# Optimization experiments

Hardware: AMD Instinct MI355X
Metric: run time of the kernel (lower is better)

Reference implementation:

```python
import jax, jax.numpy as jnp
import numpy as np

N_QUESTION = 10000
B, S = 256, 500
Q_DIM = 128
QA_DIM = 128
M = 64            # memory_size
KEY_DIM = 128
VAL_DIM = 256


def setup_inputs() -> dict:
    key = jax.random.key(0)
    ks = jax.random.split(key, 10)
    q_data = jax.random.randint(ks[0], (B, S), 0, N_QUESTION + 1)
    qa_data = jax.random.randint(ks[1], (B, S), 0, 2 * N_QUESTION + 1)
    # embedding tables with padding_idx=0 zeroed
    q_embed_w = jax.random.normal(ks[2], (N_QUESTION + 1, Q_DIM), jnp.float32) * 0.05
    q_embed_w = q_embed_w.at[0].set(0.0)
    qa_embed_w = jax.random.normal(ks[3], (2 * N_QUESTION + 1, QA_DIM), jnp.float32) * 0.05
    qa_embed_w = qa_embed_w.at[0].set(0.0)
    key_mem = jax.random.normal(ks[4], (M, KEY_DIM), jnp.float32) * (2.0 / KEY_DIM) ** 0.5
    init_value_mem = jax.random.normal(ks[5], (M, VAL_DIM), jnp.float32) * (2.0 / VAL_DIM) ** 0.5
    erase_W = jax.random.normal(ks[6], (QA_DIM, VAL_DIM), jnp.float32) * (2.0 / QA_DIM) ** 0.5
    erase_b = jnp.zeros((VAL_DIM,), jnp.float32)
    add_W = jax.random.normal(ks[7], (QA_DIM, VAL_DIM), jnp.float32) * (2.0 / QA_DIM) ** 0.5
    add_b = jnp.zeros((VAL_DIM,), jnp.float32)
    return {
        "q_data": q_data, "qa_data": qa_data,
        "q_embed_w": q_embed_w, "qa_embed_w": qa_embed_w,
        "key_mem": key_mem, "init_value_mem": init_value_mem,
        "erase_W": erase_W, "erase_b": erase_b,
        "add_W": add_W, "add_b": add_b,
    }


def reference(q_data, qa_data, q_embed_w, qa_embed_w, key_mem, init_value_mem,
              erase_W, erase_b, add_W, add_b):
    q_emb = q_embed_w[q_data]     # [B,S,Qd]
    qa_emb = qa_embed_w[qa_data]  # [B,S,QAd]
    write_mask = (q_data >= 1).astype(jnp.float32)  # [B,S]

    Mv0 = jnp.broadcast_to(init_value_mem[None], (q_data.shape[0], M, VAL_DIM))

    def step(Mv, xs):
        q_t, qa_t, m_t = xs  # [B,Qd], [B,QAd], [B]
        # attention over memory slots
        w = jax.nn.softmax(q_t @ key_mem.T, axis=-1)           # [B,M]
        read = jnp.einsum('bm,bmd->bd', w, Mv)                 # [B,D]
        erase = jax.nn.sigmoid(qa_t @ erase_W + erase_b)       # [B,D]
        add = jnp.tanh(qa_t @ add_W + add_b)                   # [B,D]
        new_Mv = Mv * (1.0 - w[:, :, None] * erase[:, None, :]) \
                 + w[:, :, None] * add[:, None, :]
        Mv = jnp.where(m_t[:, None, None] > 0, new_Mv, Mv)
        return Mv, read

    xs = (jnp.swapaxes(q_emb, 0, 1), jnp.swapaxes(qa_emb, 0, 1),
          jnp.swapaxes(write_mask, 0, 1))
    _, reads = jax.lax.scan(step, Mv0, xs)        # reads: [S,B,D]
    reads = jnp.swapaxes(reads, 0, 1)             # [B,S,D]
    # shift right by one timestep, zero-pad first step
    out = jnp.concatenate([jnp.zeros_like(reads[:, :1]), reads[:, :-1]], axis=1)
    return out
```

## Files before the change

kernel.cpp:

```cpp
#include <hip/hip_runtime.h>
#include <math.h>

#define B_     256
#define S_     500
#define QD_    128
#define M_     64
#define VD_    256
#define CH_    16
#define NQ_    10000
#define NQA_   20000
#define WROWS  (NQ_ + 1)
#define EAROWS (NQA_ + 1)

__global__ void kT_kernel(const float* __restrict__ key_mem, float4* __restrict__ kTq)
{
    int i = blockIdx.x * 256 + threadIdx.x;
    if (i < 32 * 64) {
        int m  = i & 63;
        int k4 = i >> 6;
        kTq[i] = *reinterpret_cast<const float4*>(&key_mem[m * QD_ + k4 * 4]);
    }
}

__global__ __launch_bounds__(256) void wtab_kernel(
    const float*  __restrict__ q_embed_w,
    const float4* __restrict__ kTq,
    float*        __restrict__ wtab)
{
    __shared__ float4 q4[16][32];

    const int tid = threadIdx.x;
    const int r0  = blockIdx.x * 16;

    for (int i = tid; i < 512; i += 256) {
        int row = i >> 5, k4 = i & 31;
        int r   = r0 + row; if (r > NQ_) r = NQ_;
        q4[row][k4] = *reinterpret_cast<const float4*>(
            &q_embed_w[(size_t)r * QD_ + k4 * 4]);
    }
    __syncthreads();

    const int wave = tid >> 6, lane = tid & 63;
    const int rr = wave * 4;

    float s0 = 0.f, s1 = 0.f, s2 = 0.f, s3 = 0.f;
    for (int k4 = 0; k4 < 32; ++k4) {
        float4 kv = kTq[k4 * 64 + lane];
        float4 a0 = q4[rr + 0][k4];
        float4 a1 = q4[rr + 1][k4];
        float4 a2 = q4[rr + 2][k4];
        float4 a3 = q4[rr + 3][k4];
        s0 = fmaf(a0.x, kv.x, s0); s0 = fmaf(a0.y, kv.y, s0);
        s0 = fmaf(a0.z, kv.z, s0); s0 = fmaf(a0.w, kv.w, s0);
        s1 = fmaf(a1.x, kv.x, s1); s1 = fmaf(a1.y, kv.y, s1);
        s1 = fmaf(a1.z, kv.z, s1); s1 = fmaf(a1.w, kv.w, s1);
        s2 = fmaf(a2.x, kv.x, s2); s2 = fmaf(a2.y, kv.y, s2);
        s2 = fmaf(a2.z, kv.z, s2); s2 = fmaf(a2.w, kv.w, s2);
        s3 = fmaf(a3.x, kv.x, s3); s3 = fmaf(a3.y, kv.y, s3);
        s3 = fmaf(a3.z, kv.z, s3); s3 = fmaf(a3.w, kv.w, s3);
    }

    float s[4] = { s0, s1, s2, s3 };
    #pragma unroll
    for (int j = 0; j < 4; ++j) {
        float mx = s[j];
        #pragma unroll
        for (int off = 32; off; off >>= 1) mx = fmaxf(mx, __shfl_xor(mx, off));
        float e = __expf(s[j] - mx);
        float sum = e;
        #pragma unroll
        for (int off = 32; off; off >>= 1) sum += __shfl_xor(sum, off);
        if (r0 + rr + j < WROWS)
            wtab[(size_t)(r0 + rr + j) * 64 + lane] = e / sum;
    }
}

__global__ __launch_bounds__(512) void eatab_kernel(
    const float* __restrict__ qa_embed_w,
    const float* __restrict__ erase_W,
    const float* __restrict__ erase_b,
    const float* __restrict__ add_W,
    const float* __restrict__ add_b,
    float*       __restrict__ eatab)
{
    __shared__ float4 qa4[16][32];

    const int tid = threadIdx.x;
    const int r0  = blockIdx.x * 16;

    {
        int row = tid >> 5, k4 = tid & 31;
        int r   = r0 + row; if (r > NQA_) r = NQA_;
        qa4[row][k4] = *reinterpret_cast<const float4*>(
            &qa_embed_w[(size_t)r * QD_ + k4 * 4]);
    }
    __syncthreads();

    const int  c   = tid & 255;
    const bool isE = tid < 256;
    const float* Wp = isE ? erase_W : add_W;

    float acc[16];
    #pragma unroll
    for (int r = 0; r < 16; ++r) acc[r] = 0.f;

    for (int k4 = 0; k4 < 32; ++k4) {
        float w0 = Wp[(size_t)(k4 * 4 + 0) * 256 + c];
        float w1 = Wp[(size_t)(k4 * 4 + 1) * 256 + c];
        float w2 = Wp[(size_t)(k4 * 4 + 2) * 256 + c];
        float w3 = Wp[(size_t)(k4 * 4 + 3) * 256 + c];
        #pragma unroll
        for (int r = 0; r < 16; ++r) {
            float4 qv = qa4[r][k4];
            acc[r] = fmaf(qv.x, w0, acc[r]);
            acc[r] = fmaf(qv.y, w1, acc[r]);
            acc[r] = fmaf(qv.z, w2, acc[r]);
            acc[r] = fmaf(qv.w, w3, acc[r]);
        }
    }

    const float bias = isE ? erase_b[c] : add_b[c];
    #pragma unroll
    for (int r = 0; r < 16; ++r) {
        float x = acc[r] + bias;
        float y;
        if (isE) {
            y = 1.f / (1.f + __expf(-x));
        } else {
            float t  = __expf(-2.f * fabsf(x));
            float ta = (1.f - t) / (1.f + t);
            y = (x < 0.f) ? -ta : ta;
        }
        if (r0 + r < EAROWS)
            eatab[(size_t)(r0 + r) * 512 + tid] = y;
    }
}

__global__ __launch_bounds__(512, 1) void scan_kernel(
    const int*   __restrict__ q_data,
    const int*   __restrict__ qa_data,
    const float* __restrict__ init_mv,
    const float* __restrict__ wtab,
    const float* __restrict__ eatab,
    float*       __restrict__ out)
{
    __shared__ float w_lds[2][CH_ * 64];
    __shared__ int   qrow[S_];
    __shared__ int   qarow[S_];

    const int b   = blockIdx.x;
    const int tid = threadIdx.x;
    const int col = (tid >> 2) * 2;
    const int ms  = tid & 3;
    const int mo  = ms * 16;

    for (int i = tid; i < S_; i += 512) {
        qrow[i]  = q_data[b * S_ + i];
        qarow[i] = qa_data[b * S_ + i];
    }
    __syncthreads();

    float4 mv0[4], mv1[4];
    #pragma unroll
    for (int q = 0; q < 4; ++q) {
        float2 i0 = *reinterpret_cast<const float2*>(&init_mv[(mo + q * 4 + 0) * VD_ + col]);
        float2 i1 = *reinterpret_cast<const float2*>(&init_mv[(mo + q * 4 + 1) * VD_ + col]);
        float2 i2 = *reinterpret_cast<const float2*>(&init_mv[(mo + q * 4 + 2) * VD_ + col]);
        float2 i3 = *reinterpret_cast<const float2*>(&init_mv[(mo + q * 4 + 3) * VD_ + col]);
        mv0[q].x = i0.x; mv1[q].x = i0.y;
        mv0[q].y = i1.x; mv1[q].y = i1.y;
        mv0[q].z = i2.x; mv1[q].z = i2.y;
        mv0[q].w = i3.x; mv1[q].w = i3.y;
    }
    if (ms == 0)
        *reinterpret_cast<float2*>(&out[(size_t)b * S_ * VD_ + col]) = make_float2(0.f, 0.f);

    if (tid < 256) {
        int wstep = tid >> 4, wq4 = tid & 15;
        *reinterpret_cast<float4*>(&w_lds[0][wstep * 64 + wq4 * 4]) =
            *reinterpret_cast<const float4*>(&wtab[(size_t)qrow[wstep] * 64 + wq4 * 4]);
    }
    float2 ec[CH_], ac[CH_];
    #pragma unroll
    for (int j = 0; j < CH_; ++j) {
        const float* rowp = &eatab[(size_t)qarow[j] * 512 + col];
        ec[j] = *reinterpret_cast<const float2*>(&rowp[0]);
        ac[j] = *reinterpret_cast<const float2*>(&rowp[256]);
    }
    __syncthreads();

    const int nch = (S_ + CH_ - 1) / CH_;
    for (int c = 0; c < nch; ++c) {
        const int  tb   = c * CH_;
        const int  full = (S_ - tb >= CH_);
        const int  buf  = c & 1;
        const bool hn   = (c + 1 < nch);

        float4 rw;
        float2 en[CH_], an[CH_];
        if (hn) {
            if (tid < 256) {
                int wstep = tid >> 4, wq4 = tid & 15;
                int st = tb + CH_ + wstep; if (st >= S_) st = S_ - 1;
                rw = *reinterpret_cast<const float4*>(
                    &wtab[(size_t)qrow[st] * 64 + wq4 * 4]);
            }
            #pragma unroll
            for (int j = 0; j < CH_; ++j) {
                int st = tb + CH_ + j; if (st >= S_) st = S_ - 1;
                const float* rowp = &eatab[(size_t)qarow[st] * 512 + col];
                en[j] = *reinterpret_cast<const float2*>(&rowp[0]);
                an[j] = *reinterpret_cast<const float2*>(&rowp[256]);
            }
        }

        float* outp = &out[((size_t)b * S_ + tb + 1) * VD_ + col];

        #define STEP_BODY(tt)                                                       \
        {                                                                           \
            const int  t  = tb + (tt);                                              \
            const bool wr = qrow[t] >= 1;                                           \
            const float em0 = wr ? ec[(tt)].x : 0.f;                                \
            const float am0 = wr ? ac[(tt)].x : 0.f;                                \
            const float em1 = wr ? ec[(tt)].y : 0.f;                                \
            const float am1 = wr ? ac[(tt)].y : 0.f;                                \
            const float* wrow = &w_lds[buf][(tt) * 64 + mo];                        \
            float r0a = 0.f, r0b = 0.f, r1a = 0.f, r1b = 0.f;                       \
            _Pragma("unroll")                                                       \
            for (int q = 0; q < 4; ++q) {                                           \
                float4 wq = *reinterpret_cast<const float4*>(wrow + q * 4);         \
                float4 v0 = mv0[q];                                                 \
                float4 v1 = mv1[q];                                                 \
                r0a = fmaf(wq.x, v0.x, r0a); r0b = fmaf(wq.y, v0.y, r0b);           \
                r0a = fmaf(wq.z, v0.z, r0a); r0b = fmaf(wq.w, v0.w, r0b);           \
                r1a = fmaf(wq.x, v1.x, r1a); r1b = fmaf(wq.y, v1.y, r1b);           \
                r1a = fmaf(wq.z, v1.z, r1a); r1b = fmaf(wq.w, v1.w, r1b);           \
                mv0[q].x = fmaf(wq.x, fmaf(-em0, v0.x, am0), v0.x);                 \
                mv0[q].y = fmaf(wq.y, fmaf(-em0, v0.y, am0), v0.y);                 \
                mv0[q].z = fmaf(wq.z, fmaf(-em0, v0.z, am0), v0.z);                 \
                mv0[q].w = fmaf(wq.w, fmaf(-em0, v0.w, am0), v0.w);                 \
                mv1[q].x = fmaf(wq.x, fmaf(-em1, v1.x, am1), v1.x);                 \
                mv1[q].y = fmaf(wq.y, fmaf(-em1, v1.y, am1), v1.y);                 \
                mv1[q].z = fmaf(wq.z, fmaf(-em1, v1.z, am1), v1.z);                 \
                mv1[q].w = fmaf(wq.w, fmaf(-em1, v1.w, am1), v1.w);                 \
            }                                                                       \
            float rd0 = r0a + r0b;                                                  \
            rd0 += __shfl_xor(rd0, 1);                                              \
            rd0 += __shfl_xor(rd0, 2);                                              \
            float rd1 = r1a + r1b;                                                  \
            rd1 += __shfl_xor(rd1, 1);                                              \
            rd1 += __shfl_xor(rd1, 2);                                              \
            if (ms == 0 && (t + 1 < S_))                                            \
                *reinterpret_cast<float2*>(&outp[(size_t)(tt) * VD_]) =             \
                    make_float2(rd0, rd1);                                          \
        }

        if (full) {
            #pragma unroll
            for (int tt = 0; tt < CH_; ++tt) STEP_BODY(tt)
        } else {
            #pragma unroll
            for (int tt = 0; tt < CH_; ++tt) {
                if (tb + tt < S_) STEP_BODY(tt)
            }
        }
        #undef STEP_BODY

        if (hn) {
            if (tid < 256) {
                int wstep = tid >> 4, wq4 = tid & 15;
                *reinterpret_cast<float4*>(&w_lds[buf ^ 1][wstep * 64 + wq4 * 4]) = rw;
            }
            #pragma unroll
            for (int j = 0; j < CH_; ++j) { ec[j] = en[j]; ac[j] = an[j]; }
        }
        __syncthreads();
    }
}

extern "C" void kernel_launch(void* const* d_in, const int* in_sizes, int n_in,
                              void* d_out, int out_size, void* d_ws, size_t ws_size,
                              hipStream_t stream)
{
    const int*   q_data  = (const int*)  d_in[0];
    const int*   qa_data = (const int*)  d_in[1];
    const float* q_emb   = (const float*)d_in[2];
    const float* qa_emb  = (const float*)d_in[3];
    const float* key_mem = (const float*)d_in[4];
    const float* init_mv = (const float*)d_in[5];
    const float* erase_W = (const float*)d_in[6];
    const float* erase_b = (const float*)d_in[7];
    const float* add_W   = (const float*)d_in[8];
    const float* add_b   = (const float*)d_in[9];
    float* out = (float*)d_out;

    char* ws = (char*)d_ws;
    float4* kTq = (float4*)ws;
    size_t off = (size_t)2048 * sizeof(float4);
    float* wtab = (float*)(ws + off);
    off += (size_t)WROWS * 64 * sizeof(float);
    off = (off + 255) & ~(size_t)255;
    float* eatab = (float*)(ws + off);
    off += (size_t)EAROWS * 512 * sizeof(float);

    kT_kernel<<<dim3(8), dim3(256), 0, stream>>>(key_mem, kTq);
    wtab_kernel<<<dim3((WROWS + 15) / 16), dim3(256), 0, stream>>>(
        q_emb, kTq, wtab);
    eatab_kernel<<<dim3((EAROWS + 15) / 16), dim3(512), 0, stream>>>(
        qa_emb, erase_W, erase_b, add_W, add_b, eatab);
    scan_kernel<<<dim3(B_), dim3(512), 0, stream>>>(
        q_data, qa_data, init_mv, wtab, eatab, out);
}
```

Baseline: 369.8 us.

## Stage next chunk's weights and erase/add rows directly into LDS via async global_load_lds

Replaces the register-prefetch of the next chunk's attention weights and erase/add vectors with direct global-to-LDS loads (global_load_lds, 16 bytes per lane) into double-buffered shared arrays. The step body then reads erase/add pairs from LDS. This frees the 64 prefetch registers per thread and the copy-back loop at chunk end, and lets the loads proceed asynchronously during compute. The cost is extra LDS traffic per step, about 64KB more shared memory, and a reliance on the implicit wait before the barrier to keep the buffers correct.

```diff
diff --git a/kernel.cpp b/kernel.cpp
--- a/kernel.cpp
+++ b/kernel.cpp
@@ -11,6 +11,15 @@
 #define NQA_   20000
 #define WROWS  (NQ_ + 1)
 #define EAROWS (NQA_ + 1)
+
+typedef unsigned int u32;
+
+__device__ __forceinline__ void gload_lds16(const float* g, float* l)
+{
+    __builtin_amdgcn_global_load_lds(
+        (const __attribute__((address_space(1))) u32*)(const void*)g,
+        (__attribute__((address_space(3))) u32*)(void*)l, 16, 0, 0);
+}
 
 __global__ void kT_kernel(const float* __restrict__ key_mem, float4* __restrict__ kTq)
 {
@@ -136,6 +145,28 @@
     }
 }
 
+__device__ __forceinline__ void stage_chunk(
+    int tb, int tid,
+    const int* __restrict__ qrow, const int* __restrict__ qarow,
+    const float* __restrict__ wtab, const float* __restrict__ eatab,
+    float* wbuf, float* ebuf, float* abuf)
+{
+    if (tid < 256) {
+        int st = tb + (tid >> 4); if (st >= S_) st = S_ - 1;
+        gload_lds16(&wtab[(size_t)qrow[st] * 64 + (tid & 15) * 4],
+                    &wbuf[(tid & ~63) * 4]);
+    }
+    #pragma unroll
+    for (int j = 0; j < 2; ++j) {
+        const int idx = tid + 512 * j;
+        int st = tb + (idx >> 6); if (st >= S_) st = S_ - 1;
+        const int cq = (idx & 63) * 4;
+        const float* rowp = &eatab[(size_t)qarow[st] * 512];
+        gload_lds16(&rowp[cq],       &ebuf[(idx & ~63) * 4]);
+        gload_lds16(&rowp[256 + cq], &abuf[(idx & ~63) * 4]);
+    }
+}
+
 __global__ __launch_bounds__(512, 1) void scan_kernel(
     const int*   __restrict__ q_data,
     const int*   __restrict__ qa_data,
@@ -145,6 +176,8 @@
     float*       __restrict__ out)
 {
     __shared__ float w_lds[2][CH_ * 64];
+    __shared__ float e_lds[2][CH_ * VD_];
+    __shared__ float a_lds[2][CH_ * VD_];
     __shared__ int   qrow[S_];
     __shared__ int   qarow[S_];
 
@@ -159,6 +192,9 @@
         qarow[i] = qa_data[b * S_ + i];
     }
     __syncthreads();
+
+    stage_chunk(0, tid, qrow, qarow, wtab, eatab,
+                w_lds[0], e_lds[0], a_lds[0]);
 
     float4 mv0[4], mv1[4];
     #pragma unroll
@@ -175,18 +211,6 @@
     if (ms == 0)
         *reinterpret_cast<float2*>(&out[(size_t)b * S_ * VD_ + col]) = make_float2(0.f, 0.f);
 
-    if (tid < 256) {
-        int wstep = tid >> 4, wq4 = tid & 15;
-        *reinterpret_cast<float4*>(&w_lds[0][wstep * 64 + wq4 * 4]) =
-            *reinterpret_cast<const float4*>(&wtab[(size_t)qrow[wstep] * 64 + wq4 * 4]);
-    }
-    float2 ec[CH_], ac[CH_];
-    #pragma unroll
-    for (int j = 0; j < CH_; ++j) {
-        const float* rowp = &eatab[(size_t)qarow[j] * 512 + col];
-        ec[j] = *reinterpret_cast<const float2*>(&rowp[0]);
-        ac[j] = *reinterpret_cast<const float2*>(&rowp[256]);
-    }
     __syncthreads();
 
     const int nch = (S_ + CH_ - 1) / CH_;
@@ -196,23 +220,9 @@
         const int  buf  = c & 1;
         const bool hn   = (c + 1 < nch);
 
-        float4 rw;
-        float2 en[CH_], an[CH_];
-        if (hn) {
-            if (tid < 256) {
-                int wstep = tid >> 4, wq4 = tid & 15;
-                int st = tb + CH_ + wstep; if (st >= S_) st = S_ - 1;
-                rw = *reinterpret_cast<const float4*>(
-                    &wtab[(size_t)qrow[st] * 64 + wq4 * 4]);
-            }
-            #pragma unroll
-            for (int j = 0; j < CH_; ++j) {
-                int st = tb + CH_ + j; if (st >= S_) st = S_ - 1;
-                const float* rowp = &eatab[(size_t)qarow[st] * 512 + col];
-                en[j] = *reinterpret_cast<const float2*>(&rowp[0]);
-                an[j] = *reinterpret_cast<const float2*>(&rowp[256]);
-            }
-        }
+        if (hn)
+            stage_chunk(tb + CH_, tid, qrow, qarow, wtab, eatab,
+                        w_lds[buf ^ 1], e_lds[buf ^ 1], a_lds[buf ^ 1]);
 
         float* outp = &out[((size_t)b * S_ + tb + 1) * VD_ + col];
 
@@ -220,10 +230,12 @@
         {                                                                           \
             const int  t  = tb + (tt);                                              \
             const bool wr = qrow[t] >= 1;                                           \
-            const float em0 = wr ? ec[(tt)].x : 0.f;                                \
-            const float am0 = wr ? ac[(tt)].x : 0.f;                                \
-            const float em1 = wr ? ec[(tt)].y : 0.f;                                \
-            const float am1 = wr ? ac[(tt)].y : 0.f;                                \
+            float2 ev = *reinterpret_cast<const float2*>(&e_lds[buf][(tt) * VD_ + col]); \
+            float2 av = *reinterpret_cast<const float2*>(&a_lds[buf][(tt) * VD_ + col]); \
+            const float em0 = wr ? ev.x : 0.f;                                      \
+            const float am0 = wr ? av.x : 0.f;                                      \
+            const float em1 = wr ? ev.y : 0.f;                                      \
+            const float am1 = wr ? av.y : 0.f;                                      \
             const float* wrow = &w_lds[buf][(tt) * 64 + mo];                        \
             float r0a = 0.f, r0b = 0.f, r1a = 0.f, r1b = 0.f;                       \
             _Pragma("unroll")                                                       \
@@ -266,14 +278,6 @@
         }
         #undef STEP_BODY
 
-        if (hn) {
-            if (tid < 256) {
-                int wstep = tid >> 4, wq4 = tid & 15;
-                *reinterpret_cast<float4*>(&w_lds[buf ^ 1][wstep * 64 + wq4 * 4]) = rw;
-            }
-            #pragma unroll
-            for (int j = 0; j < CH_; ++j) { ec[j] = en[j]; ac[j] = an[j]; }
-        }
         __syncthreads();
     }
 }
```

Result: faster. 332.9 us (-10.0%).
